# Optimization experiments

Measured on AMD Instinct MI355X. Metric: run time of the kernel, lower is better.

## Reference

```python
import jax, jax.numpy as jnp
import numpy as np

NEG_SLOPE = 0.2  # PyG GATConv default negative_slope


def _gat_layer(x, src, dst, W, a_s, a_d, b, heads, ch):
    N = x.shape[0]
    h = (x @ W).reshape(N, heads, ch)                      # [N,H,C]
    al_s = jnp.sum(h * a_s[None], axis=-1)                 # [N,H]
    al_d = jnp.sum(h * a_d[None], axis=-1)                 # [N,H]
    e = jax.nn.leaky_relu(al_s[src] + al_d[dst], NEG_SLOPE)  # [E,H]
    m = jax.ops.segment_max(e, dst, num_segments=N)        # segment-softmax (stable)
    ex = jnp.exp(e - jax.lax.stop_gradient(m)[dst])
    denom = jax.ops.segment_sum(ex, dst, num_segments=N)
    alpha = ex / (denom[dst] + 1e-16)                      # [E,H]
    msg = h[src] * alpha[..., None]                        # [E,H,C]
    out = jax.ops.segment_sum(msg, dst, num_segments=N)    # [N,H,C]
    return out.reshape(N, heads * ch) + b


def _add_self_loops(edge_index, N):
    loop = jnp.arange(N, dtype=edge_index.dtype)
    src = jnp.concatenate([edge_index[0], loop])
    dst = jnp.concatenate([edge_index[1], loop])
    return src, dst


def gat_forward(x, edge_index, batch, W1, a_src1, a_dst1, b1, W2, a_src2, a_dst2, b2, W3, a_src3, a_dst3, b3, num_graphs=512):
    N = x.shape[0]
    src, dst = _add_self_loops(edge_index, N)
    x = jax.nn.relu(_gat_layer(x, src, dst, W1, a_src1, a_dst1, b1, 4, 64))
    x = jax.nn.relu(_gat_layer(x, src, dst, W2, a_src2, a_dst2, b2, 4, 64))
    x = _gat_layer(x, src, dst, W3, a_src3, a_dst3, b3, 1, 32)
    # global_mean_pool
    sums = jax.ops.segment_sum(x, batch, num_segments=num_graphs)
    cnt = jax.ops.segment_sum(jnp.ones((N,), x.dtype), batch, num_segments=num_graphs)
    return sums / jnp.maximum(cnt, 1.0)[:, None]


def setup_inputs() -> dict:
    key = jax.random.key(0)
    ks = jax.random.split(key, 16)
    N, E, G = 50000, 800000, 512
    IN, HID, H, OUT = 775, 64, 4, 32
    s = 0.05
    return {
        "x": jax.random.normal(ks[0], (N, IN), jnp.float32),
        "edge_index": jax.random.randint(ks[1], (2, E), 0, N, jnp.int32),
        "batch": jnp.sort(jax.random.randint(ks[2], (N,), 0, G, jnp.int32)),
        "W1": jax.random.normal(ks[3], (IN, H * HID), jnp.float32) * s,
        "a_src1": jax.random.normal(ks[4], (H, HID), jnp.float32) * s,
        "a_dst1": jax.random.normal(ks[5], (H, HID), jnp.float32) * s,
        "b1": jnp.zeros((H * HID,), jnp.float32),
        "W2": jax.random.normal(ks[6], (H * HID, H * HID), jnp.float32) * s,
        "a_src2": jax.random.normal(ks[7], (H, HID), jnp.float32) * s,
        "a_dst2": jax.random.normal(ks[8], (H, HID), jnp.float32) * s,
        "b2": jnp.zeros((H * HID,), jnp.float32),
        "W3": jax.random.normal(ks[9], (H * HID, OUT), jnp.float32) * s,
        "a_src3": jax.random.normal(ks[10], (1, OUT), jnp.float32) * s,
        "a_dst3": jax.random.normal(ks[11], (1, OUT), jnp.float32) * s,
        "b3": jnp.zeros((OUT,), jnp.float32),
    }


def reference(x, edge_index, batch, W1, a_src1, a_dst1, b1, W2, a_src2, a_dst2, b2, W3, a_src3, a_dst3, b3):
    return gat_forward(x, edge_index, batch, W1, a_src1, a_dst1, b1, W2, a_src2, a_dst2, b2, W3, a_src3, a_dst3, b3)
```

## Files before the change

### kernel.cpp

```cpp
#include <hip/hip_runtime.h>
#include <hip/hip_bf16.h>

typedef unsigned short u16;
typedef __attribute__((ext_vector_type(4))) unsigned short u16x4;
typedef __attribute__((ext_vector_type(8))) unsigned short u16x8;
typedef __attribute__((ext_vector_type(8))) short bf16x8;
typedef __attribute__((ext_vector_type(4))) float f32x4;

__device__ __forceinline__ u16 f2bs(float f) {
    union { float f; unsigned int u; } x; x.f = f;
    unsigned int r = x.u + 0x7FFFu + ((x.u >> 16) & 1u);
    return (u16)(r >> 16);
}
__device__ __forceinline__ float bs2f(u16 u) {
    union { unsigned int u; float f; } x; x.u = ((unsigned int)u) << 16; return x.f;
}
__device__ __forceinline__ float lrelu(float e) { return e >= 0.f ? e : 0.2f * e; }

__device__ __forceinline__ unsigned cvtpk(float lo, float hi) {
    unsigned r;
    asm("v_cvt_pk_bf16_f32 %0, %1, %2" : "=v"(r) : "v"(lo), "v"(hi));
    return r;
}

__device__ __forceinline__ void glds16(const void* g, void* l) {
    __builtin_amdgcn_global_load_lds(
        (const __attribute__((address_space(1))) unsigned int*)g,
        (__attribute__((address_space(3))) unsigned int*)l, 16, 0, 0);
}

__global__ void deg_kernel(const int* __restrict__ dst, int* __restrict__ deg, int E) {
    int i = blockIdx.x * 256 + threadIdx.x;
    if (i < E) atomicAdd(&deg[dst[i]], 1);
}

__global__ __launch_bounds__(1024) void scan_local(const int* __restrict__ deg,
        int* __restrict__ ptr, int* __restrict__ bsum, int N) {
    __shared__ int wsum[16];
    const int t = threadIdx.x, i = blockIdx.x * 1024 + t;
    const int lane = t & 63, w = t >> 6;
    int v = (i < N) ? deg[i] : 0;
    int x = v;
    #pragma unroll
    for (int off = 1; off < 64; off <<= 1) { int y = __shfl_up(x, off); if (lane >= off) x += y; }
    if (lane == 63) wsum[w] = x;
    __syncthreads();
    if (w == 0) {
        int s = (lane < 16) ? wsum[lane] : 0;
        #pragma unroll
        for (int off = 1; off < 16; off <<= 1) { int y = __shfl_up(s, off); if (lane >= off) s += y; }
        if (lane < 16) wsum[lane] = s;
    }
    __syncthreads();
    int incl = x + (w > 0 ? wsum[w - 1] : 0);
    if (i < N) ptr[i + 1] = incl;
    if (t == 0) bsum[blockIdx.x] = wsum[15];
}

__global__ __launch_bounds__(64) void scan_carry(int* __restrict__ bsum, int nb) {
    int t = threadIdx.x;
    int v = (t < nb) ? bsum[t] : 0;
    int x = v;
    #pragma unroll
    for (int off = 1; off < 64; off <<= 1) { int y = __shfl_up(x, off); if (t >= off) x += y; }
    if (t < nb) bsum[t] = x - v;
}

__global__ __launch_bounds__(1024) void scan_final(const int* __restrict__ deg,
        int* __restrict__ ptr, int* __restrict__ cur, const int* __restrict__ bsum, int N) {
    int i = blockIdx.x * 1024 + threadIdx.x;
    if (i == 0) ptr[0] = 0;
    if (i < N) {
        int p = ptr[i + 1] + bsum[blockIdx.x];
        ptr[i + 1] = p;
        cur[i] = p - deg[i];
    }
}

__global__ void fill_kernel(const int* __restrict__ src, const int* __restrict__ dst,
        int* __restrict__ cur, int* __restrict__ csr, int E) {
    int i = blockIdx.x * 256 + threadIdx.x;
    if (i < E) { int p = atomicAdd(&cur[dst[i]], 1); csr[p] = src[i]; }
}

__global__ void bounds_kernel(const int* __restrict__ batch, int* __restrict__ gstart,
        int N, int G) {
    int i = blockIdx.x * 256 + threadIdx.x;
    if (i > N) return;
    if (i == 0) {
        int b0 = batch[0];
        for (int g = 0; g <= b0; g++) gstart[g] = 0;
    } else if (i == N) {
        int bl = batch[N - 1];
        for (int g = bl + 1; g <= G; g++) gstart[g] = N;
    } else {
        int b = batch[i], bp = batch[i - 1];
        for (int g = bp + 1; g <= b; g++) gstart[g] = i;
    }
}

__global__ void transpose_w(const float* __restrict__ W, u16* __restrict__ Wt,
        int K, int Nn, int KT) {
    int idx = blockIdx.x * 256 + threadIdx.x;
    if (idx >= Nn * KT) return;
    int n = idx / KT, k = idx - n * KT;
    Wt[(size_t)n * KT + k] = (k < K) ? f2bs(W[(size_t)k * Nn + n]) : (u16)0;
}

__global__ __launch_bounds__(256) void tail_kernel(const float* __restrict__ x,
        float* __restrict__ xtail, int N) {
    int idx = blockIdx.x * 256 + threadIdx.x;
    if (idx >= N * 32) return;
    int n = idx >> 5, j = idx & 31;
    xtail[idx] = (768 + j < 775) ? x[(size_t)n * 775 + 768 + j] : 0.f;
}

__global__ __launch_bounds__(256) void gemm_glds_f32(
        const float* __restrict__ A, int lda, int M,
        const float* __restrict__ Atail,
        const u16* __restrict__ B, int ldb,
        u16* __restrict__ C, int ldc) {
    __shared__ float Aldsf[2][128][32];
    __shared__ u16   Blds[2][128][32];
    const int t = threadIdx.x;
    const int col0 = blockIdx.x * 128;
    const int row0 = blockIdx.y * 128;
    const int wid = t >> 6, lane = t & 63;
    const int wm = wid >> 1, wn = wid & 1;
    const int quad = lane >> 4, l16 = lane & 15;

    f32x4 acc[4][4];
    f32x4 z = {0.f, 0.f, 0.f, 0.f};
    #pragma unroll
    for (int i = 0; i < 4; i++)
        #pragma unroll
        for (int j = 0; j < 4; j++) acc[i][j] = z;

    const int trb = wid * 32 + (lane >> 2);
    const int arl = lane >> 3;
    const int asg = lane & 7;

    auto stage = [&](int buf, int kt) {
        const int k0 = kt << 5;
        #pragma unroll
        for (int c = 0; c < 2; c++) {
            const int tr = trb + c * 16;
            const int ks = ((lane & 3) ^ ((tr >> 1) & 3)) * 8;
            glds16(B + (size_t)(col0 + tr) * ldb + k0 + ks, &Blds[buf][wid * 32 + c * 16][0]);
        }
        #pragma unroll
        for (int c = 0; c < 4; c++) {
            const int rt = wid * 32 + c * 8 + arl;
            int gra = row0 + rt; if (gra > M - 1) gra = M - 1;
            const int sg = (asg ^ ((rt & 3) << 1)) * 4;
            const float* src = (kt < 24) ? (A + (size_t)gra * lda + k0 + sg)
                                         : (Atail + (size_t)gra * 32 + sg);
            glds16(src, &Aldsf[buf][wid * 32 + c * 8][0]);
        }
    };

    const int kTiles = 25;
    stage(0, 0);
    __syncthreads();
    int cur = 0;
    for (int kt = 0; kt < kTiles; ++kt) {
        if (kt + 1 < kTiles) stage(cur ^ 1, kt + 1);
        bf16x8 af[4], bfr[4];
        #pragma unroll
        for (int it = 0; it < 4; it++) {
            const int r = wm * 64 + it * 16 + l16;
            const int go = ((2 * quad) ^ ((r & 3) << 1)) * 4;
            const f32x4 lo = *(const f32x4*)&Aldsf[cur][r][go];
            const f32x4 hi = *(const f32x4*)&Aldsf[cur][r][go + 4];
            union { unsigned u[4]; bf16x8 v; } uu;
            uu.u[0] = cvtpk(lo[0], lo[1]);
            uu.u[1] = cvtpk(lo[2], lo[3]);
            uu.u[2] = cvtpk(hi[0], hi[1]);
            uu.u[3] = cvtpk(hi[2], hi[3]);
            af[it] = uu.v;
        }
        #pragma unroll
        for (int jt = 0; jt < 4; jt++) {
            const int r = wn * 64 + jt * 16 + l16;
            bfr[jt] = *(const bf16x8*)&Blds[cur][r][(quad ^ ((r >> 1) & 3)) * 8];
        }
        #pragma unroll
        for (int it = 0; it < 4; it++)
            #pragma unroll
            for (int jt = 0; jt < 4; jt++)
                acc[it][jt] = __builtin_amdgcn_mfma_f32_16x16x32_bf16(af[it], bfr[jt], acc[it][jt], 0, 0, 0);
        __syncthreads();
        cur ^= 1;
    }
    #pragma unroll
    for (int it = 0; it < 4; it++) {
        int gr0 = row0 + wm * 64 + it * 16 + quad * 4;
        #pragma unroll
        for (int jt = 0; jt < 4; jt++) {
            int gc = col0 + wn * 64 + jt * 16 + l16;
            #pragma unroll
            for (int r = 0; r < 4; r++) {
                int gr = gr0 + r;
                if (gr < M) C[(size_t)gr * ldc + gc] = f2bs(acc[it][jt][r]);
            }
        }
    }
}

__global__ __launch_bounds__(256) void gemm_glds(
        const u16* __restrict__ A, int lda, int M, int K,
        const u16* __restrict__ B, int ldb,
        u16* __restrict__ C, int ldc) {
    __shared__ u16 Alds[2][128][32];
    __shared__ u16 Blds[2][128][32];
    const int t = threadIdx.x;
    const int col0 = blockIdx.x * 128;
    const int row0 = blockIdx.y * 128;
    const int wid = t >> 6, lane = t & 63;
    const int wm = wid >> 1, wn = wid & 1;
    const int quad = lane >> 4, l16 = lane & 15;

    f32x4 acc[4][4];
    f32x4 z = {0.f, 0.f, 0.f, 0.f};
    #pragma unroll
    for (int i = 0; i < 4; i++)
        #pragma unroll
        for (int j = 0; j < 4; j++) acc[i][j] = z;

    const int trb = wid * 32 + (lane >> 2);

    auto stage = [&](int buf, int kt) {
        const int k0 = kt << 5;
        #pragma unroll
        for (int c = 0; c < 2; c++) {
            const int tr = trb + c * 16;
            const int ks = ((lane & 3) ^ ((tr >> 1) & 3)) * 8;
            int gra = row0 + tr; if (gra > M - 1) gra = M - 1;
            glds16(A + (size_t)gra * lda + k0 + ks, &Alds[buf][wid * 32 + c * 16][0]);
            glds16(B + (size_t)(col0 + tr) * ldb + k0 + ks, &Blds[buf][wid * 32 + c * 16][0]);
        }
    };

    const int kTiles = K >> 5;
    stage(0, 0);
    __syncthreads();
    int cur = 0;
    for (int kt = 0; kt < kTiles; ++kt) {
        if (kt + 1 < kTiles) stage(cur ^ 1, kt + 1);
        bf16x8 af[4], bfr[4];
        #pragma unroll
        for (int it = 0; it < 4; it++) {
            const int r = wm * 64 + it * 16 + l16;
            af[it] = *(const bf16x8*)&Alds[cur][r][(quad ^ ((r >> 1) & 3)) * 8];
        }
        #pragma unroll
        for (int jt = 0; jt < 4; jt++) {
            const int r = wn * 64 + jt * 16 + l16;
            bfr[jt] = *(const bf16x8*)&Blds[cur][r][(quad ^ ((r >> 1) & 3)) * 8];
        }
        #pragma unroll
        for (int it = 0; it < 4; it++)
            #pragma unroll
            for (int jt = 0; jt < 4; jt++)
                acc[it][jt] = __builtin_amdgcn_mfma_f32_16x16x32_bf16(af[it], bfr[jt], acc[it][jt], 0, 0, 0);
        __syncthreads();
        cur ^= 1;
    }
    #pragma unroll
    for (int it = 0; it < 4; it++) {
        int gr0 = row0 + wm * 64 + it * 16 + quad * 4;
        #pragma unroll
        for (int jt = 0; jt < 4; jt++) {
            int gc = col0 + wn * 64 + jt * 16 + l16;
            #pragma unroll
            for (int r = 0; r < 4; r++) {
                int gr = gr0 + r;
                if (gr < M) C[(size_t)gr * ldc + gc] = f2bs(acc[it][jt][r]);
            }
        }
    }
}

__global__ __launch_bounds__(256) void gemm32(
        const u16* __restrict__ A, int lda, int M, int K,
        const u16* __restrict__ B, int ldb, float* __restrict__ C) {
    __shared__ u16 Alds[128][40];
    __shared__ u16 Blds[32][40];
    const int t = threadIdx.x;
    const int row0 = blockIdx.x * 128;
    const int wid = t >> 6, lane = t & 63;
    const int quad = lane >> 4, l16 = lane & 15;
    f32x4 acc[2][2];
    f32x4 z = {0.f, 0.f, 0.f, 0.f};
    acc[0][0] = z; acc[0][1] = z; acc[1][0] = z; acc[1][1] = z;
    const int kTiles = K >> 5;
    for (int kt = 0; kt < kTiles; ++kt) {
        const int k0 = kt << 5;
        #pragma unroll
        for (int c = 0; c < 2; c++) {
            int ch = t + c * 256;
            int r = ch >> 2, cp = (ch & 3) * 8;
            int gr = row0 + r;
            u16x8 v = {0,0,0,0,0,0,0,0};
            if (gr < M) v = *(const u16x8*)(A + (size_t)gr * lda + k0 + cp);
            *(u16x8*)&Alds[r][cp] = v;
        }
        if (t < 128) {
            int r = t >> 2, cp = (t & 3) * 8;
            *(u16x8*)&Blds[r][cp] = *(const u16x8*)(B + (size_t)r * ldb + k0 + cp);
        }
        __syncthreads();
        bf16x8 af[2], bfr[2];
        #pragma unroll
        for (int it = 0; it < 2; it++) af[it] = *(const bf16x8*)&Alds[wid * 32 + it * 16 + l16][quad * 8];
        #pragma unroll
        for (int jt = 0; jt < 2; jt++) bfr[jt] = *(const bf16x8*)&Blds[jt * 16 + l16][quad * 8];
        #pragma unroll
        for (int it = 0; it < 2; it++)
            #pragma unroll
            for (int jt = 0; jt < 2; jt++)
                acc[it][jt] = __builtin_amdgcn_mfma_f32_16x16x32_bf16(af[it], bfr[jt], acc[it][jt], 0, 0, 0);
        __syncthreads();
    }
    #pragma unroll
    for (int it = 0; it < 2; it++) {
        int gr0 = row0 + wid * 32 + it * 16 + quad * 4;
        #pragma unroll
        for (int jt = 0; jt < 2; jt++) {
            int gc = jt * 16 + l16;
            #pragma unroll
            for (int r = 0; r < 4; r++) {
                int gr = gr0 + r;
                if (gr < M) C[(size_t)gr * 32 + gc] = acc[it][jt][r];
            }
        }
    }
}

__global__ __launch_bounds__(256) void al_kernel(const u16* __restrict__ h,
        const float* __restrict__ a_s, const float* __restrict__ a_d,
        float* __restrict__ als, float* __restrict__ ald, int N) {
    const int t = threadIdx.x, wid = t >> 6, lane = t & 63;
    const f32x4 as4 = *(const f32x4*)&a_s[lane * 4];
    const f32x4 ad4 = *(const f32x4*)&a_d[lane * 4];
    #pragma unroll
    for (int u = 0; u < 2; u++) {
        const int n = blockIdx.x * 8 + wid * 2 + u;
        if (n >= N) return;
        const u16x4 hv = *(const u16x4*)&h[(size_t)n * 256 + lane * 4];
        float ps = 0.f, pd = 0.f;
        #pragma unroll
        for (int c = 0; c < 4; c++) {
            const float f = bs2f(hv[c]);
            ps = fmaf(f, as4[c], ps);
            pd = fmaf(f, ad4[c], pd);
        }
        #pragma unroll
        for (int off = 8; off >= 1; off >>= 1) {
            ps += __shfl_xor(ps, off, 16);
            pd += __shfl_xor(pd, off, 16);
        }
        if ((lane & 15) == 0) {
            als[n * 4 + (lane >> 4)] = ps;
            ald[n * 4 + (lane >> 4)] = pd;
        }
    }
}

__global__ __launch_bounds__(256) void al3_kernel(const float* __restrict__ h3,
        const float* __restrict__ a_s, const float* __restrict__ a_d,
        float* __restrict__ als, float* __restrict__ ald, int N) {
    int t = threadIdx.x, wid = t >> 6, lane = t & 63;
    int c = lane & 31, half = lane >> 5;
    float as = a_s[c], ad = a_d[c];
    int n = blockIdx.x * 8 + wid * 2 + half;
    if (n >= N) return;
    float hv = h3[(size_t)n * 32 + c];
    float ps = hv * as, pd = hv * ad;
    for (int off = 16; off >= 1; off >>= 1) { ps += __shfl_down(ps, off, 32); pd += __shfl_down(pd, off, 32); }
    if (c == 0) { als[n] = ps; ald[n] = pd; }
}

__global__ __launch_bounds__(256) void agg_kernel(const u16* __restrict__ hbuf,
        const float* __restrict__ als, const float* __restrict__ ald,
        const int* __restrict__ ptr, const int* __restrict__ csr,
        const float* __restrict__ bias, u16* __restrict__ act, int N) {
    __shared__ float al_lds[4][64][4];
    __shared__ int   s_lds[4][64];
    const int t = threadIdx.x, wid = t >> 6, lane = t & 63;
    const int i = blockIdx.x * 4 + wid;
    if (i >= N) return;
    const int start = ptr[i], end = ptr[i + 1];
    const int deg = end - start;
    const int col8 = lane & 31;
    const int half = lane >> 5;
    const int head8 = col8 >> 3;

    const f32x4 aldv = *(const f32x4*)&ald[(size_t)i * 4];
    const f32x4 alsv = *(const f32x4*)&als[(size_t)i * 4];
    f32x4 eself;
    #pragma unroll
    for (int hh = 0; hh < 4; hh++) eself[hh] = lrelu(alsv[hh] + aldv[hh]);

    float acc[8];
    f32x4 mx, inv;

    if (deg <= 64) {
        int sreg = 0;
        f32x4 ev;
        #pragma unroll
        for (int hh = 0; hh < 4; hh++) ev[hh] = -1e30f;
        if (lane < deg) {
            sreg = csr[start + lane];
            const f32x4 a = *(const f32x4*)&als[(size_t)sreg * 4];
            #pragma unroll
            for (int hh = 0; hh < 4; hh++) ev[hh] = lrelu(a[hh] + aldv[hh]);
        }
        #pragma unroll
        for (int hh = 0; hh < 4; hh++) mx[hh] = fmaxf(eself[hh], ev[hh]);
        #pragma unroll
        for (int off = 32; off >= 1; off >>= 1) {
            #pragma unroll
            for (int hh = 0; hh < 4; hh++) mx[hh] = fmaxf(mx[hh], __shfl_xor(mx[hh], off));
        }
        f32x4 sm, av;
        #pragma unroll
        for (int hh = 0; hh < 4; hh++) {
            av[hh] = (lane < deg) ? expf(ev[hh] - mx[hh]) : 0.f;
            sm[hh] = av[hh] + ((lane == 0) ? expf(eself[hh] - mx[hh]) : 0.f);
        }
        #pragma unroll
        for (int off = 32; off >= 1; off >>= 1) {
            #pragma unroll
            for (int hh = 0; hh < 4; hh++) sm[hh] += __shfl_xor(sm[hh], off);
        }
        #pragma unroll
        for (int hh = 0; hh < 4; hh++) inv[hh] = 1.f / (sm[hh] + 1e-16f);
        #pragma unroll
        for (int hh = 0; hh < 4; hh++) av[hh] *= inv[hh];
        *(f32x4*)&al_lds[wid][lane][0] = av;
        s_lds[wid][lane] = sreg;

        const u16x8 hrs = *(const u16x8*)&hbuf[(size_t)i * 256 + col8 * 8];
        const float aself = expf(eself[head8] - mx[head8]) * inv[head8];
        #pragma unroll
        for (int c = 0; c < 8; c++) acc[c] = (half == 0) ? aself * bs2f(hrs[c]) : 0.f;

        int k = half;
        for (; k + 6 < deg; k += 8) {
            const int s0 = s_lds[wid][k],     s1 = s_lds[wid][k + 2];
            const int s2 = s_lds[wid][k + 4], s3 = s_lds[wid][k + 6];
            const float a0 = al_lds[wid][k][head8],     a1 = al_lds[wid][k + 2][head8];
            const float a2 = al_lds[wid][k + 4][head8], a3 = al_lds[wid][k + 6][head8];
            const u16x8 h0 = *(const u16x8*)&hbuf[(size_t)s0 * 256 + col8 * 8];
            const u16x8 h1 = *(const u16x8*)&hbuf[(size_t)s1 * 256 + col8 * 8];
            const u16x8 h2 = *(const u16x8*)&hbuf[(size_t)s2 * 256 + col8 * 8];
            const u16x8 h3v = *(const u16x8*)&hbuf[(size_t)s3 * 256 + col8 * 8];
            #pragma unroll
            for (int c = 0; c < 8; c++) {
                acc[c] = fmaf(a0, bs2f(h0[c]), acc[c]);
                acc[c] = fmaf(a1, bs2f(h1[c]), acc[c]);
                acc[c] = fmaf(a2, bs2f(h2[c]), acc[c]);
                acc[c] = fmaf(a3, bs2f(h3v[c]), acc[c]);
            }
        }
        for (; k < deg; k += 2) {
            const int s = s_lds[wid][k];
            const float a = al_lds[wid][k][head8];
            const u16x8 hr = *(const u16x8*)&hbuf[(size_t)s * 256 + col8 * 8];
            #pragma unroll
            for (int c = 0; c < 8; c++) acc[c] = fmaf(a, bs2f(hr[c]), acc[c]);
        }
    } else {
        mx = eself;
        for (int j = start + lane; j < end; j += 64) {
            int s = csr[j];
            const f32x4 a = *(const f32x4*)&als[(size_t)s * 4];
            #pragma unroll
            for (int hh = 0; hh < 4; hh++) mx[hh] = fmaxf(mx[hh], lrelu(a[hh] + aldv[hh]));
        }
        #pragma unroll
        for (int off = 32; off >= 1; off >>= 1) {
            #pragma unroll
            for (int hh = 0; hh < 4; hh++) mx[hh] = fmaxf(mx[hh], __shfl_xor(mx[hh], off));
        }
        f32x4 sm;
        #pragma unroll
        for (int hh = 0; hh < 4; hh++) sm[hh] = (lane == 0) ? expf(eself[hh] - mx[hh]) : 0.f;
        for (int j = start + lane; j < end; j += 64) {
            int s = csr[j];
            const f32x4 a = *(const f32x4*)&als[(size_t)s * 4];
            #pragma unroll
            for (int hh = 0; hh < 4; hh++) sm[hh] += expf(lrelu(a[hh] + aldv[hh]) - mx[hh]);
        }
        #pragma unroll
        for (int off = 32; off >= 1; off >>= 1) {
            #pragma unroll
            for (int hh = 0; hh < 4; hh++) sm[hh] += __shfl_xor(sm[hh], off);
        }
        #pragma unroll
        for (int hh = 0; hh < 4; hh++) inv[hh] = 1.f / (sm[hh] + 1e-16f);

        const u16x8 hrs = *(const u16x8*)&hbuf[(size_t)i * 256 + col8 * 8];
        const float aself = expf(eself[head8] - mx[head8]) * inv[head8];
        #pragma unroll
        for (int c = 0; c < 8; c++) acc[c] = (half == 0) ? aself * bs2f(hrs[c]) : 0.f;

        for (int base = start; base < end; base += 64) {
            const int n64 = min(64, end - base);
            const int j = base + lane;
            int sreg = 0;
            if (j < end) {
                sreg = csr[j];
                const f32x4 a = *(const f32x4*)&als[(size_t)sreg * 4];
                f32x4 alpha;
                #pragma unroll
                for (int hh = 0; hh < 4; hh++)
                    alpha[hh] = expf(lrelu(a[hh] + aldv[hh]) - mx[hh]) * inv[hh];
                *(f32x4*)&al_lds[wid][lane][0] = alpha;
            }
            s_lds[wid][lane] = sreg;
            for (int k = half; k < n64; k += 2) {
                const int s = s_lds[wid][k];
                const float a = al_lds[wid][k][head8];
                const u16x8 hr = *(const u16x8*)&hbuf[(size_t)s * 256 + col8 * 8];
                #pragma unroll
                for (int c = 0; c < 8; c++) acc[c] = fmaf(a, bs2f(hr[c]), acc[c]);
            }
        }
    }

    #pragma unroll
    for (int c = 0; c < 8; c++) acc[c] += __shfl_down(acc[c], 32);
    if (half == 0) {
        const f32x4 bv0 = *(const f32x4*)&bias[col8 * 8];
        const f32x4 bv1 = *(const f32x4*)&bias[col8 * 8 + 4];
        u16x8 o;
        #pragma unroll
        for (int c = 0; c < 4; c++) o[c] = f2bs(fmaxf(acc[c] + bv0[c], 0.f));
        #pragma unroll
        for (int c = 4; c < 8; c++) o[c] = f2bs(fmaxf(acc[c] + bv1[c - 4], 0.f));
        *(u16x8*)&act[(size_t)i * 256 + col8 * 8] = o;
    }
}

__global__ __launch_bounds__(256) void agg3_kernel(const float* __restrict__ h3,
        const float* __restrict__ als, const float* __restrict__ ald,
        const int* __restrict__ ptr, const int* __restrict__ csr,
        const float* __restrict__ bias, float* __restrict__ out_n, int N) {
    __shared__ float a_lds[4][64];
    __shared__ int   s_lds3[4][64];
    const int t = threadIdx.x, wid = t >> 6, lane = t & 63;
    const int col = lane & 31, half = lane >> 5;
    const int i = blockIdx.x * 4 + wid;
    if (i >= N) return;
    const int start = ptr[i], end = ptr[i + 1];
    const int deg = end - start;
    const float aldv = ald[i];
    const float e0 = lrelu(als[i] + aldv);
    float acc = 0.f;

    if (deg <= 64) {
        int sreg = 0; float ev = -1e30f;
        if (lane < deg) { sreg = csr[start + lane]; ev = lrelu(als[sreg] + aldv); }
        float mx = fmaxf(e0, ev);
        #pragma unroll
        for (int off = 32; off >= 1; off >>= 1) mx = fmaxf(mx, __shfl_xor(mx, off));
        float ex = (lane < deg) ? expf(ev - mx) : 0.f;
        float sm = ex + ((lane == 0) ? expf(e0 - mx) : 0.f);
        #pragma unroll
        for (int off = 32; off >= 1; off >>= 1) sm += __shfl_xor(sm, off);
        const float inv = 1.f / (sm + 1e-16f);
        a_lds[wid][lane] = ex * inv;
        s_lds3[wid][lane] = sreg;
        if (half == 0) acc = expf(e0 - mx) * inv * h3[(size_t)i * 32 + col];

        int k = half;
        for (; k + 6 < deg; k += 8) {
            const int s0 = s_lds3[wid][k],     s1 = s_lds3[wid][k + 2];
            const int s2 = s_lds3[wid][k + 4], s3 = s_lds3[wid][k + 6];
            const float a0 = a_lds[wid][k],     a1 = a_lds[wid][k + 2];
            const float a2 = a_lds[wid][k + 4], a3 = a_lds[wid][k + 6];
            const float v0 = h3[(size_t)s0 * 32 + col];
            const float v1 = h3[(size_t)s1 * 32 + col];
            const float v2 = h3[(size_t)s2 * 32 + col];
            const float v3 = h3[(size_t)s3 * 32 + col];
            acc = fmaf(a0, v0, acc); acc = fmaf(a1, v1, acc);
            acc = fmaf(a2, v2, acc); acc = fmaf(a3, v3, acc);
        }
        for (; k < deg; k += 2)
            acc = fmaf(a_lds[wid][k], h3[(size_t)s_lds3[wid][k] * 32 + col], acc);
    } else {
        float mx = e0;
        for (int j = start + lane; j < end; j += 64)
            mx = fmaxf(mx, lrelu(als[csr[j]] + aldv));
        #pragma unroll
        for (int off = 32; off >= 1; off >>= 1) mx = fmaxf(mx, __shfl_xor(mx, off));
        float sm = (lane == 0) ? expf(e0 - mx) : 0.f;
        for (int j = start + lane; j < end; j += 64)
            sm += expf(lrelu(als[csr[j]] + aldv) - mx);
        #pragma unroll
        for (int off = 32; off >= 1; off >>= 1) sm += __shfl_xor(sm, off);
        const float inv = 1.f / (sm + 1e-16f);
        if (half == 0) acc = expf(e0 - mx) * inv * h3[(size_t)i * 32 + col];
        for (int base = start; base < end; base += 64) {
            const int n64 = min(64, end - base);
            const int j = base + lane;
            int sreg = 0; float av = 0.f;
            if (j < end) {
                sreg = csr[j];
                av = expf(lrelu(als[sreg] + aldv) - mx) * inv;
            }
            a_lds[wid][lane] = av;
            s_lds3[wid][lane] = sreg;
            for (int k = half; k < n64; k += 2)
                acc = fmaf(a_lds[wid][k], h3[(size_t)s_lds3[wid][k] * 32 + col], acc);
        }
    }

    acc += __shfl_down(acc, 32);
    if (half == 0)
        out_n[(size_t)i * 32 + col] = acc + bias[col];
}

__global__ __launch_bounds__(256) void pool_kernel(const float* __restrict__ out_n,
        const int* __restrict__ gstart, float* __restrict__ out, int G) {
    const int t = threadIdx.x, wid = t >> 6, lane = t & 63;
    const int col = lane & 31, half = lane >> 5;
    const int g = blockIdx.x * 4 + wid;
    if (g >= G) return;
    const int s = gstart[g], e = gstart[g + 1];
    float acc = 0.f;
    int r = s + half;
    for (; r + 6 < e; r += 8) {
        acc += out_n[(size_t)r * 32 + col];
        acc += out_n[(size_t)(r + 2) * 32 + col];
        acc += out_n[(size_t)(r + 4) * 32 + col];
        acc += out_n[(size_t)(r + 6) * 32 + col];
    }
    for (; r < e; r += 2) acc += out_n[(size_t)r * 32 + col];
    acc += __shfl_down(acc, 32);
    if (half == 0)
        out[g * 32 + col] = acc / fmaxf((float)(e - s), 1.f);
}

extern "C" void kernel_launch(void* const* d_in, const int* in_sizes, int n_in,
                              void* d_out, int out_size, void* d_ws, size_t ws_size,
                              hipStream_t stream) {
    const int N = 50000, E = 800000, G = 512;
    const float* x    = (const float*)d_in[0];
    const int*   ei   = (const int*)d_in[1];
    const int*   batch= (const int*)d_in[2];
    const float* W1   = (const float*)d_in[3];
    const float* as1  = (const float*)d_in[4];
    const float* ad1  = (const float*)d_in[5];
    const float* b1   = (const float*)d_in[6];
    const float* W2   = (const float*)d_in[7];
    const float* as2  = (const float*)d_in[8];
    const float* ad2  = (const float*)d_in[9];
    const float* b2   = (const float*)d_in[10];
    const float* W3   = (const float*)d_in[11];
    const float* as3  = (const float*)d_in[12];
    const float* ad3  = (const float*)d_in[13];
    const float* b3   = (const float*)d_in[14];
    const int* esrc = ei;
    const int* edst = ei + E;

    char* base = (char*)d_ws; size_t off = 0;
    auto alloc = [&](size_t bytes) -> void* {
        void* p = base + off; off = (off + bytes + 255) & ~(size_t)255; return p;
    };
    u16*   hbuf = (u16*)  alloc((size_t)N * 256 * 2);
    u16*   act  = (u16*)  alloc((size_t)N * 256 * 2);
    float* h3   = (float*)alloc((size_t)N * 32 * 4);
    float* als  = (float*)alloc((size_t)N * 4 * 4);
    float* ald  = (float*)alloc((size_t)N * 4 * 4);
    int*   deg  = (int*)  alloc((size_t)N * 4);
    int*   ptr  = (int*)  alloc((size_t)(N + 1) * 4);
    int*   cur  = (int*)  alloc((size_t)N * 4);
    int*   csr  = (int*)  alloc((size_t)E * 4);
    u16*   Wt   = (u16*)  alloc((size_t)256 * 800 * 2);
    int*   bsum = (int*)  alloc((size_t)64 * 4);
    float* out_n= (float*)alloc((size_t)N * 32 * 4);
    int*   gstart=(int*)  alloc((size_t)(G + 1) * 4);
    float* xtail= (float*)alloc((size_t)N * 32 * 4);

    hipMemsetAsync(deg, 0, (size_t)N * 4, stream);

    const int nb = (N + 1023) / 1024;
    deg_kernel<<<(E + 255) / 256, 256, 0, stream>>>(edst, deg, E);
    scan_local<<<nb, 1024, 0, stream>>>(deg, ptr, bsum, N);
    scan_carry<<<1, 64, 0, stream>>>(bsum, nb);
    scan_final<<<nb, 1024, 0, stream>>>(deg, ptr, cur, bsum, N);
    fill_kernel<<<(E + 255) / 256, 256, 0, stream>>>(esrc, edst, cur, csr, E);
    bounds_kernel<<<(N + 256) / 256, 256, 0, stream>>>(batch, gstart, N, G);

    dim3 gemmGrid(2, (N + 127) / 128);
    const int aggGrid = (N + 3) / 4;
    transpose_w<<<(256 * 800 + 255) / 256, 256, 0, stream>>>(W1, Wt, 775, 256, 800);
    tail_kernel<<<(N * 32 + 255) / 256, 256, 0, stream>>>(x, xtail, N);
    gemm_glds_f32<<<gemmGrid, 256, 0, stream>>>(x, 775, N, xtail, Wt, 800, hbuf, 256);
    al_kernel<<<(N + 7) / 8, 256, 0, stream>>>(hbuf, as1, ad1, als, ald, N);
    agg_kernel<<<aggGrid, 256, 0, stream>>>(hbuf, als, ald, ptr, csr, b1, act, N);
    transpose_w<<<(256 * 256 + 255) / 256, 256, 0, stream>>>(W2, Wt, 256, 256, 256);
    gemm_glds<<<gemmGrid, 256, 0, stream>>>(act, 256, N, 256, Wt, 256, hbuf, 256);
    al_kernel<<<(N + 7) / 8, 256, 0, stream>>>(hbuf, as2, ad2, als, ald, N);
    agg_kernel<<<aggGrid, 256, 0, stream>>>(hbuf, als, ald, ptr, csr, b2, act, N);
    transpose_w<<<(32 * 256 + 255) / 256, 256, 0, stream>>>(W3, Wt, 256, 32, 256);
    gemm32<<<(N + 127) / 128, 256, 0, stream>>>(act, 256, N, 256, Wt, 256, h3);
    al3_kernel<<<(N + 7) / 8, 256, 0, stream>>>(h3, as3, ad3, als, ald, N);
    agg3_kernel<<<aggGrid, 256, 0, stream>>>(h3, als, ald, ptr, csr, b3, out_n, N);
    pool_kernel<<<(G + 3) / 4, 256, 0, stream>>>(out_n, gstart, (float*)d_out, G);
}
```

Baseline: 613.3 us.

## Triple-buffer GEMM LDS staging with explicit vmcnt waits and single barrier

Both bf16 MFMA GEMM kernels move from double-buffered to triple-buffered LDS staging, prefetching two K tiles ahead. The two __syncthreads per iteration become one explicit s_waitcnt vmcnt plus s_barrier, so global-to-LDS loads for later tiles stay in flight during compute. This aims to hide global load latency and cut barrier stalls, at the cost of more LDS per block (72KB for the f32-A kernel), which may lower occupancy.

```diff
diff --git a/kernel.cpp b/kernel.cpp
--- a/kernel.cpp
+++ b/kernel.cpp
@@ -120,8 +120,8 @@
         const float* __restrict__ Atail,
         const u16* __restrict__ B, int ldb,
         u16* __restrict__ C, int ldc) {
-    __shared__ float Aldsf[2][128][32];
-    __shared__ u16   Blds[2][128][32];
+    __shared__ float Aldsf[3][128][32];
+    __shared__ u16   Blds[3][128][32];
     const int t = threadIdx.x;
     const int col0 = blockIdx.x * 128;
     const int row0 = blockIdx.y * 128;
@@ -158,20 +158,14 @@
             glds16(src, &Aldsf[buf][wid * 32 + c * 8][0]);
         }
     };
-
-    const int kTiles = 25;
-    stage(0, 0);
-    __syncthreads();
-    int cur = 0;
-    for (int kt = 0; kt < kTiles; ++kt) {
-        if (kt + 1 < kTiles) stage(cur ^ 1, kt + 1);
+    auto compute = [&](int buf) {
         bf16x8 af[4], bfr[4];
         #pragma unroll
         for (int it = 0; it < 4; it++) {
             const int r = wm * 64 + it * 16 + l16;
             const int go = ((2 * quad) ^ ((r & 3) << 1)) * 4;
-            const f32x4 lo = *(const f32x4*)&Aldsf[cur][r][go];
-            const f32x4 hi = *(const f32x4*)&Aldsf[cur][r][go + 4];
+            const f32x4 lo = *(const f32x4*)&Aldsf[buf][r][go];
+            const f32x4 hi = *(const f32x4*)&Aldsf[buf][r][go + 4];
             union { unsigned u[4]; bf16x8 v; } uu;
             uu.u[0] = cvtpk(lo[0], lo[1]);
             uu.u[1] = cvtpk(lo[2], lo[3]);
@@ -182,16 +176,32 @@
         #pragma unroll
         for (int jt = 0; jt < 4; jt++) {
             const int r = wn * 64 + jt * 16 + l16;
-            bfr[jt] = *(const bf16x8*)&Blds[cur][r][(quad ^ ((r >> 1) & 3)) * 8];
+            bfr[jt] = *(const bf16x8*)&Blds[buf][r][(quad ^ ((r >> 1) & 3)) * 8];
         }
         #pragma unroll
         for (int it = 0; it < 4; it++)
             #pragma unroll
             for (int jt = 0; jt < 4; jt++)
                 acc[it][jt] = __builtin_amdgcn_mfma_f32_16x16x32_bf16(af[it], bfr[jt], acc[it][jt], 0, 0, 0);
-        __syncthreads();
-        cur ^= 1;
-    }
+    };
+
+    const int kTiles = 25;
+    stage(0, 0);
+    stage(1, 1);
+    for (int kt = 0; kt < kTiles - 1; ++kt) {
+        asm volatile("s_waitcnt vmcnt(6)" ::: "memory");
+        __builtin_amdgcn_sched_barrier(0);
+        __builtin_amdgcn_s_barrier();
+        __builtin_amdgcn_sched_barrier(0);
+        if (kt + 2 < kTiles) stage((kt + 2) % 3, kt + 2);
+        compute(kt % 3);
+    }
+    asm volatile("s_waitcnt vmcnt(0)" ::: "memory");
+    __builtin_amdgcn_sched_barrier(0);
+    __builtin_amdgcn_s_barrier();
+    __builtin_amdgcn_sched_barrier(0);
+    compute((kTiles - 1) % 3);
+
     #pragma unroll
     for (int it = 0; it < 4; it++) {
         int gr0 = row0 + wm * 64 + it * 16 + quad * 4;
@@ -211,8 +221,8 @@
         const u16* __restrict__ A, int lda, int M, int K,
         const u16* __restrict__ B, int ldb,
         u16* __restrict__ C, int ldc) {
-    __shared__ u16 Alds[2][128][32];
-    __shared__ u16 Blds[2][128][32];
+    __shared__ u16 Alds[3][128][32];
+    __shared__ u16 Blds[3][128][32];
     const int t = threadIdx.x;
     const int col0 = blockIdx.x * 128;
     const int row0 = blockIdx.y * 128;
@@ -240,32 +250,42 @@
             glds16(B + (size_t)(col0 + tr) * ldb + k0 + ks, &Blds[buf][wid * 32 + c * 16][0]);
         }
     };
+    auto compute = [&](int buf) {
+        bf16x8 af[4], bfr[4];
+        #pragma unroll
+        for (int it = 0; it < 4; it++) {
+            const int r = wm * 64 + it * 16 + l16;
+            af[it] = *(const bf16x8*)&Alds[buf][r][(quad ^ ((r >> 1) & 3)) * 8];
+        }
+        #pragma unroll
+        for (int jt = 0; jt < 4; jt++) {
+            const int r = wn * 64 + jt * 16 + l16;
+            bfr[jt] = *(const bf16x8*)&Blds[buf][r][(quad ^ ((r >> 1) & 3)) * 8];
+        }
+        #pragma unroll
+        for (int it = 0; it < 4; it++)
+            #pragma unroll
+            for (int jt = 0; jt < 4; jt++)
+                acc[it][jt] = __builtin_amdgcn_mfma_f32_16x16x32_bf16(af[it], bfr[jt], acc[it][jt], 0, 0, 0);
+    };
 
     const int kTiles = K >> 5;
     stage(0, 0);
-    __syncthreads();
-    int cur = 0;
-    for (int kt = 0; kt < kTiles; ++kt) {
-        if (kt + 1 < kTiles) stage(cur ^ 1, kt + 1);
-        bf16x8 af[4], bfr[4];
-        #pragma unroll
-        for (int it = 0; it < 4; it++) {
-            const int r = wm * 64 + it * 16 + l16;
-            af[it] = *(const bf16x8*)&Alds[cur][r][(quad ^ ((r >> 1) & 3)) * 8];
-        }
-        #pragma unroll
-        for (int jt = 0; jt < 4; jt++) {
-            const int r = wn * 64 + jt * 16 + l16;
-            bfr[jt] = *(const bf16x8*)&Blds[cur][r][(quad ^ ((r >> 1) & 3)) * 8];
-        }
-        #pragma unroll
-        for (int it = 0; it < 4; it++)
-            #pragma unroll
-            for (int jt = 0; jt < 4; jt++)
-                acc[it][jt] = __builtin_amdgcn_mfma_f32_16x16x32_bf16(af[it], bfr[jt], acc[it][jt], 0, 0, 0);
-        __syncthreads();
-        cur ^= 1;
-    }
+    stage(1, 1);
+    for (int kt = 0; kt < kTiles - 1; ++kt) {
+        asm volatile("s_waitcnt vmcnt(4)" ::: "memory");
+        __builtin_amdgcn_sched_barrier(0);
+        __builtin_amdgcn_s_barrier();
+        __builtin_amdgcn_sched_barrier(0);
+        if (kt + 2 < kTiles) stage((kt + 2) % 3, kt + 2);
+        compute(kt % 3);
+    }
+    asm volatile("s_waitcnt vmcnt(0)" ::: "memory");
+    __builtin_amdgcn_sched_barrier(0);
+    __builtin_amdgcn_s_barrier();
+    __builtin_amdgcn_sched_barrier(0);
+    compute((kTiles - 1) % 3);
+
     #pragma unroll
     for (int it = 0; it < 4; it++) {
         int gr0 = row0 + wm * 64 + it * 16 + quad * 4;
```

Measured after the change: 617.3 us. About the same (+0.7%).
